# Kernel tuning notes

Hardware: AMD Instinct MI355X
Metric: run time of the kernel (lower is better)

Reference implementation:

```python
import jax, jax.numpy as jnp
import numpy as np
from jax import lax

B, N, C = 8, 8192, 64
ODR, K, OUT = 4, 32, 128
S = N // ODR
EPS = 1e-5


def _lbr(h, W, b, g, be):
    # h: [M, K, Cin] -> linear -> BN (training-mode batch stats over (M,K) per channel) -> relu
    y = jnp.einsum('mki,oi->mko', h, W) + b
    mean = y.mean(axis=(0, 1))
    var = ((y - mean) ** 2).mean(axis=(0, 1))  # biased var, as torch BN uses for normalization
    y = (y - mean) * lax.rsqrt(var + EPS) * g + be
    return jax.nn.relu(y)


def setup_inputs() -> dict:
    key = jax.random.key(0)
    ks = jax.random.split(key, 12)
    x = jax.random.normal(ks[0], (B, N, C), dtype=jnp.float32)
    coor = jax.random.normal(ks[1], (B, N, 3), dtype=jnp.float32)
    indx = jax.random.permutation(ks[2], N)[:S]  # like torch.randperm(N)[:S]
    w1 = jax.random.normal(ks[3], (OUT, 2 * C), dtype=jnp.float32) * (2 * C) ** -0.5
    b1 = jax.random.normal(ks[4], (OUT,), dtype=jnp.float32) * 0.01
    g1 = jax.random.uniform(ks[5], (OUT,), dtype=jnp.float32, minval=0.5, maxval=1.5)
    be1 = jax.random.normal(ks[6], (OUT,), dtype=jnp.float32) * 0.01
    w2 = jax.random.normal(ks[7], (OUT, OUT), dtype=jnp.float32) * OUT ** -0.5
    b2 = jax.random.normal(ks[8], (OUT,), dtype=jnp.float32) * 0.01
    g2 = jax.random.uniform(ks[9], (OUT,), dtype=jnp.float32, minval=0.5, maxval=1.5)
    be2 = jax.random.normal(ks[10], (OUT,), dtype=jnp.float32) * 0.01
    return dict(x=x, coor=coor, indx=indx, w1=w1, b1=b1, g1=g1, be1=be1,
                w2=w2, b2=b2, g2=g2, be2=be2)


def reference(x, coor, indx, w1, b1, g1, be1, w2, b2, g2, be2):
    sampled_coor = coor[:, indx, :]  # [B,S,3]
    sampled_x = x[:, indx, :]        # [B,S,C]
    # pairwise squared distances [B,S,N]
    dist = jnp.sum((coor[:, None, :, :] - sampled_coor[:, :, None, :]) ** 2, axis=-1)
    # k smallest distances == argsort(dist)[..., :K]
    _, knn_idx = lax.top_k(-dist, K)  # [B,S,K]
    knn_x = jax.vmap(lambda xb, ib: xb[ib])(x, knn_idx)  # [B,S,K,C]
    rep_x = jnp.broadcast_to(sampled_x[:, :, None, :], (x.shape[0], S, K, x.shape[2]))
    feat = jnp.concatenate([rep_x, knn_x - rep_x], axis=-1)  # [B,S,K,2C]
    feat = feat.reshape(x.shape[0] * S, K, 2 * x.shape[2])
    h = _lbr(feat, w1, b1, g1, be1)
    h = _lbr(h, w2, b2, g2, be2)
    h = h.reshape(x.shape[0], S, K, -1)
    out = jnp.max(h, axis=2)  # [B,S,OUT]
    return out, sampled_coor
```

## Files before the change

kernel.cpp:

```cpp
#include <hip/hip_runtime.h>
#include <stdint.h>


#define N_    8192
#define GPB_  16

typedef __attribute__((ext_vector_type(8))) short bf8;
typedef __attribute__((ext_vector_type(16))) float f32x16;
typedef __attribute__((ext_vector_type(2))) float f32x2;

__device__ __forceinline__ unsigned int bf1u(float f) {
  unsigned int u = __float_as_uint(f);
  return (u + 0x7fffu + ((u >> 16) & 1u)) >> 16;
}
__device__ __forceinline__ unsigned int bfpair(float lo, float hi) {
  return bf1u(lo) | (bf1u(hi) << 16);
}

__device__ __forceinline__ f32x2 pk_add(f32x2 a, f32x2 b) {
  f32x2 d;
  asm("v_pk_add_f32 %0, %1, %2" : "=v"(d) : "v"(a), "v"(b));
  return d;
}
__device__ __forceinline__ f32x2 pk_mul(f32x2 a, f32x2 b) {
  f32x2 d;
  asm("v_pk_mul_f32 %0, %1, %2" : "=v"(d) : "v"(a), "v"(b));
  return d;
}

__global__ __launch_bounds__(256) void kprep(const float* __restrict__ w1,
                                             const float* __restrict__ w2,
                                             const float* __restrict__ coor,
                                             const int* __restrict__ indx,
                                             unsigned short* __restrict__ w1b,
                                             unsigned short* __restrict__ w2b,
                                             float* __restrict__ outc,
                                             float* __restrict__ soa) {
  int e = blockIdx.x * 256 + threadIdx.x;
  if (e < 16384) {
    w1b[e] = (unsigned short)bf1u(w1[e]);
  } else if (e < 32768) {
    int e2 = e - 16384;
    w2b[e2] = (unsigned short)bf1u(w2[e2]);
  } else if (e < 81920) {
    int e2 = e - 32768;
    int bs = e2 / 3, c = e2 - bs * 3;
    int b = bs >> 11, s = bs & 2047;
    outc[e2] = coor[(b * N_ + indx[s]) * 3 + c];
  } else {
    int p = e - 81920;
    const int b = p >> 13, i = p & 8191;
    const float* src = coor + (size_t)p * 3;
    float* dst = soa + b * 24576;
    dst[i]         = src[0];
    dst[8192 + i]  = src[1];
    dst[16384 + i] = src[2];
  }
}

__global__ __launch_bounds__(256, 8) void kknn(const float* __restrict__ soa,
                                               const int* __restrict__ indx,
                                               int* __restrict__ knn) {
  __shared__ __align__(16) float4 sdist4[4 * 256];
  __shared__ float sTw[8];
  __shared__ unsigned long long cands[192];
  __shared__ int ccnt;

  const int gid = blockIdx.x;
  const int b = gid >> 11, s = gid & 2047;
  const int tid = threadIdx.x;
  const int w = tid >> 6, lane = tid & 63;
  const int hl = lane & 31;
  const float* Xb = soa + b * 24576;
  const float* Yb = Xb + 8192;
  const float* Zb = Xb + 16384;
  const int qi = indx[s];
  const float qx = Xb[qi], qy = Yb[qi], qz = Zb[qi];
  const f32x2 nqx = {-qx, -qx}, nqy = {-qy, -qy}, nqz = {-qz, -qz};

  f32x2 rd[8];
  float dmA = 3.4e38f, dmB = 3.4e38f;
#pragma unroll
  for (int it = 0; it < 8; ++it) {
    const int ofs = (it << 10) + (tid << 2);
    union { float4 f4; f32x2 h[2]; } X, Y, Z;
    X.f4 = *(const float4*)(Xb + ofs);
    Y.f4 = *(const float4*)(Yb + ofs);
    Z.f4 = *(const float4*)(Zb + ofs);
    const f32x2 dxl = pk_add(X.h[0], nqx), dyl = pk_add(Y.h[0], nqy),
                dzl = pk_add(Z.h[0], nqz);
    const f32x2 dxh = pk_add(X.h[1], nqx), dyh = pk_add(Y.h[1], nqy),
                dzh = pk_add(Z.h[1], nqz);
    const f32x2 sl =
        pk_add(pk_add(pk_mul(dxl, dxl), pk_mul(dyl, dyl)), pk_mul(dzl, dzl));
    const f32x2 sh =
        pk_add(pk_add(pk_mul(dxh, dxh), pk_mul(dyh, dyh)), pk_mul(dzh, dzh));
    dmA = fminf(fminf(sl.x, sl.y), dmA);
    dmB = fminf(fminf(sh.x, sh.y), dmB);
    if (it < 4) {
      rd[it * 2] = sl;
      rd[it * 2 + 1] = sh;
    } else {
      union { float4 f4; f32x2 h[2]; } st;
      st.h[0] = sl;
      st.h[1] = sh;
      sdist4[((it - 4) << 8) + tid] = st.f4;
    }
  }
  float dmin = fminf(dmA, dmB);
  if (tid == 0) ccnt = 0;
  if (tid < 192) cands[tid] = ~0ULL;

  float v = dmin;
#pragma unroll
  for (int k = 2; k <= 32; k <<= 1) {
#pragma unroll
    for (int j = k >> 1; j >= 1; j >>= 1) {
      const float o = __shfl_xor(v, j, 64);
      const bool dirAsc = ((hl & k) == 0);
      const bool lower = ((hl & j) == 0);
      const float lo = fminf(v, o), hi = fmaxf(v, o);
      v = (dirAsc == lower) ? lo : hi;
    }
  }
  if (hl == 3) sTw[(w << 1) + (lane >> 5)] = v;
  __syncthreads();
  const float T =
      fmaxf(fmaxf(fmaxf(sTw[0], sTw[1]), fmaxf(sTw[2], sTw[3])),
            fmaxf(fmaxf(sTw[4], sTw[5]), fmaxf(sTw[6], sTw[7])));

#pragma unroll
  for (int t = 0; t < 8; ++t) {
    const int p0 = ((t >> 1) << 10) + (tid << 2) + ((t & 1) << 1);
    const float d0 = rd[t].x, d1 = rd[t].y;
    if (d0 <= T) {
      const int pos = atomicAdd(&ccnt, 1);
      if (pos < 192)
        cands[pos] = ((unsigned long long)__float_as_uint(d0) << 32) |
                     (unsigned int)p0;
    }
    if (d1 <= T) {
      const int pos = atomicAdd(&ccnt, 1);
      if (pos < 192)
        cands[pos] = ((unsigned long long)__float_as_uint(d1) << 32) |
                     (unsigned int)(p0 + 1);
    }
  }
#pragma unroll
  for (int it = 4; it < 8; ++it) {
    const float4 d4 = sdist4[((it - 4) << 8) + tid];
    const int p0 = (it << 10) + (tid << 2);
    const float dd[4] = {d4.x, d4.y, d4.z, d4.w};
#pragma unroll
    for (int j = 0; j < 4; ++j) {
      if (dd[j] <= T) {
        const int pos = atomicAdd(&ccnt, 1);
        if (pos < 192)
          cands[pos] = ((unsigned long long)__float_as_uint(dd[j]) << 32) |
                       (unsigned int)(p0 + j);
      }
    }
  }
  __syncthreads();

  const int E = min(ccnt, 192);
  if (tid < E) {
    const unsigned long long key = cands[tid];
    int rank = 0;
    for (int j = 0; j < E; ++j) rank += (cands[j] < key) ? 1 : 0;
    if (rank < 32) knn[gid * 32 + rank] = (int)(unsigned int)key;
  }
}

template <int PHASE>
__global__ __launch_bounds__(256, 2) void kphase(
    const float* __restrict__ x, const int* __restrict__ indx,
    const int* __restrict__ knn, const float* __restrict__ b1,
    const unsigned short* __restrict__ w1b, const unsigned short* __restrict__ w2b,
    const float* __restrict__ b2, const float* __restrict__ st1,
    float* __restrict__ part, float* __restrict__ mout) {
  __shared__ __align__(16) unsigned short sxb[2][80];
  __shared__ __align__(16) unsigned short dls[2][32 * 68 + 8];
  __shared__ __align__(16) unsigned short h1[PHASE == 2 ? 2 * 32 * 136 : 8];

  const int tid = threadIdx.x;
  const int w = tid >> 6;
  const int lane = tid & 63;
  const int m = lane & 31, q2 = lane >> 5;
  const int col = (w << 5) + m;
  const int r8 = tid >> 3, c8 = (tid & 7) * 8;

  const int bb = blockIdx.x & 7;
  const int jj = blockIdx.x >> 3;
  const float* xb = x + (size_t)bb * (N_ * 64);
  const int gidbase = (bb << 11) + jj * GPB_;
  const int sbase = jj * GPB_;

  bf8 bf1[8];
#pragma unroll
  for (int t = 0; t < 8; ++t)
    bf1[t] = *(const bf8*)&w1b[col * 128 + t * 16 + q2 * 8];
  bf8 bf2[8];
  float s1 = 0.f, t1 = 0.f, b2v = 0.f;
  if constexpr (PHASE == 2) {
#pragma unroll
    for (int t = 0; t < 8; ++t)
      bf2[t] = *(const bf8*)&w2b[col * 128 + t * 16 + q2 * 8];
    s1 = st1[col];
    t1 = st1[128 + col];
    b2v = b2[col];
  }
  (void)w2b; (void)b2; (void)st1; (void)mout;
  const float b1c = b1[col];

  float sum = 0.f, ssq = 0.f;

  float4 ca_c, cc_c, ga_c, gc_c;
  {
    const int idx0 = indx[sbase];
    const int nbr0 = knn[(size_t)gidbase * 32 + r8];
    const float* c0 = xb + (size_t)idx0 * 64;
    ca_c = *(const float4*)(c0 + c8);
    cc_c = *(const float4*)(c0 + c8 + 4);
    const float* g0 = xb + (size_t)nbr0 * 64;
    ga_c = *(const float4*)(g0 + c8);
    gc_c = *(const float4*)(g0 + c8 + 4);
  }
  int idx_nxt = (GPB_ > 1) ? indx[sbase + 1] : 0;
  int nbr_nxt = (GPB_ > 1) ? knn[(size_t)(gidbase + 1) * 32 + r8] : 0;

#pragma unroll 1
  for (int g = 0; g < GPB_; ++g) {
    const int gid = gidbase + g;
    const int p = g & 1;

    float4 ca_n = ca_c, cc_n = cc_c, ga_n = ga_c, gc_n = gc_c;
    if (g + 1 < GPB_) {
      const float* cn = xb + (size_t)idx_nxt * 64;
      ca_n = *(const float4*)(cn + c8);
      cc_n = *(const float4*)(cn + c8 + 4);
      const float* gn = xb + (size_t)nbr_nxt * 64;
      ga_n = *(const float4*)(gn + c8);
      gc_n = *(const float4*)(gn + c8 + 4);
    }
    if (g + 2 < GPB_) {
      nbr_nxt = knn[(size_t)(gid + 2) * 32 + r8];
      idx_nxt = indx[sbase + g + 2];
    }

    {
      uint2 lo, hi;
      lo.x = bfpair(ga_c.x - ca_c.x, ga_c.y - ca_c.y);
      lo.y = bfpair(ga_c.z - ca_c.z, ga_c.w - ca_c.w);
      hi.x = bfpair(gc_c.x - cc_c.x, gc_c.y - cc_c.y);
      hi.y = bfpair(gc_c.z - cc_c.z, gc_c.w - cc_c.w);
      *(uint2*)&dls[p][r8 * 68 + c8] = lo;
      *(uint2*)&dls[p][r8 * 68 + c8 + 4] = hi;
    }
    if (tid < 8) {
      uint2 lo, hi;
      lo.x = bfpair(ca_c.x, ca_c.y);
      lo.y = bfpair(ca_c.z, ca_c.w);
      hi.x = bfpair(cc_c.x, cc_c.y);
      hi.y = bfpair(cc_c.z, cc_c.w);
      *(uint2*)&sxb[p][tid * 8] = lo;
      *(uint2*)&sxb[p][tid * 8 + 4] = hi;
    }
    asm volatile("s_waitcnt lgkmcnt(0)" ::: "memory");
    __builtin_amdgcn_s_barrier();

    bf8 af[8];
#pragma unroll
    for (int t = 0; t < 4; ++t) {
      union { bf8 v; uint2 u[2]; } fa;
      fa.u[0] = *(const uint2*)&sxb[p][t * 16 + q2 * 8];
      fa.u[1] = *(const uint2*)&sxb[p][t * 16 + q2 * 8 + 4];
      af[t] = fa.v;
    }
#pragma unroll
    for (int t = 0; t < 4; ++t) {
      union { bf8 v; uint2 u[2]; } fa;
      fa.u[0] = *(const uint2*)&dls[p][m * 68 + t * 16 + q2 * 8];
      fa.u[1] = *(const uint2*)&dls[p][m * 68 + t * 16 + q2 * 8 + 4];
      af[4 + t] = fa.v;
    }

    f32x16 acc;
#pragma unroll
    for (int r = 0; r < 16; ++r) acc[r] = b1c;
#pragma unroll
    for (int t = 0; t < 8; ++t)
      acc = __builtin_amdgcn_mfma_f32_32x32x16_bf16(af[t], bf1[t], acc, 0, 0, 0);

    if constexpr (PHASE == 1) {
#pragma unroll
      for (int r = 0; r < 16; ++r) {
        const float v = acc[r];
        sum += v;
        ssq = fmaf(v, v, ssq);
      }
    } else {
      const int hp = p * (32 * 136);
#pragma unroll
      for (int r = 0; r < 16; ++r) {
        const float hv = fmaxf(0.f, fmaf(acc[r], s1, t1));
        const int row = (r & 3) + ((r >> 2) << 3) + (q2 << 2);
        h1[hp + row * 136 + col] = (unsigned short)bf1u(hv);
      }
      asm volatile("s_waitcnt lgkmcnt(0)" ::: "memory");
      __builtin_amdgcn_s_barrier();

      f32x16 acc2;
#pragma unroll
      for (int r = 0; r < 16; ++r) acc2[r] = b2v;
#pragma unroll
      for (int t = 0; t < 8; ++t) {
        const bf8 a2 = *(const bf8*)&h1[hp + m * 136 + t * 16 + q2 * 8];
        acc2 = __builtin_amdgcn_mfma_f32_32x32x16_bf16(a2, bf2[t], acc2, 0, 0, 0);
      }

      float mx = -1e30f;
#pragma unroll
      for (int r = 0; r < 16; ++r) {
        const float v = acc2[r];
        sum += v;
        ssq = fmaf(v, v, ssq);
        mx = fmaxf(mx, v);
      }
      mx = fmaxf(mx, __shfl_xor(mx, 32, 64));
      if (lane < 32) mout[(size_t)gid * 128 + col] = mx;
    }

    ca_c = ca_n;
    cc_c = cc_n;
    ga_c = ga_n;
    gc_c = gc_n;
  }

  sum += __shfl_xor(sum, 32, 64);
  ssq += __shfl_xor(ssq, 32, 64);
  if (lane < 32) {
    part[blockIdx.x * 256 + col] = sum;
    part[blockIdx.x * 256 + 128 + col] = ssq;
  }
}

__global__ __launch_bounds__(256) void kred1(const float* __restrict__ part,
                                             double* __restrict__ dbuf) {
  const int blk = blockIdx.x;
  const int c = threadIdx.x;
  const float* p = part + (size_t)blk * 16 * 256 + c;
  double acc = 0.0;
#pragma unroll
  for (int r = 0; r < 16; ++r) acc += (double)p[r * 256];
  dbuf[blk * 256 + c] = acc;
}

__global__ __launch_bounds__(256) void kred2(const double* __restrict__ dbuf,
                                             const float* __restrict__ gam,
                                             const float* __restrict__ bet,
                                             float* __restrict__ st) {
  __shared__ double sS[256];
  const int c = threadIdx.x;
  double acc = 0.0;
#pragma unroll 8
  for (int i = 0; i < 64; ++i) acc += dbuf[i * 256 + c];
  sS[c] = acc;
  __syncthreads();
  if (c < 128) {
    const double Sv = sS[c], SSv = sS[128 + c];
    const double cnt = 524288.0;
    const double mean = Sv / cnt;
    const double var = SSv / cnt - mean * mean;
    const double scale = (double)gam[c] / sqrt(var + 1e-5);
    st[c] = (float)scale;
    st[128 + c] = (float)((double)bet[c] - mean * scale);
  }
}

__global__ __launch_bounds__(256) void kout(const float* __restrict__ m,
                                            const float* __restrict__ st2,
                                            float* __restrict__ out) {
  const int e4 = blockIdx.x * 256 + threadIdx.x;
  const int o0 = (e4 & 31) * 4;
  const float4 v = ((const float4*)m)[e4];
  const float4 sc = *(const float4*)&st2[o0];
  const float4 sh = *(const float4*)&st2[128 + o0];
  float4 r;
  r.x = fmaxf(0.f, fmaf(v.x, sc.x, sh.x));
  r.y = fmaxf(0.f, fmaf(v.y, sc.y, sh.y));
  r.z = fmaxf(0.f, fmaf(v.z, sc.z, sh.z));
  r.w = fmaxf(0.f, fmaf(v.w, sc.w, sh.w));
  ((float4*)out)[e4] = r;
}

extern "C" void kernel_launch(void* const* d_in, const int* in_sizes, int n_in,
                              void* d_out, int out_size, void* d_ws, size_t ws_size,
                              hipStream_t stream) {
  (void)in_sizes; (void)n_in; (void)out_size; (void)ws_size;
  const float* x    = (const float*)d_in[0];
  const float* coor = (const float*)d_in[1];
  const int*   indx = (const int*)d_in[2];
  const float* w1   = (const float*)d_in[3];
  const float* b1   = (const float*)d_in[4];
  const float* g1   = (const float*)d_in[5];
  const float* be1  = (const float*)d_in[6];
  const float* w2   = (const float*)d_in[7];
  const float* b2   = (const float*)d_in[8];
  const float* g2   = (const float*)d_in[9];
  const float* be2  = (const float*)d_in[10];
  float* out = (float*)d_out;

  char* ws = (char*)d_ws;
  int*            knn   = (int*)(ws + 0);
  float*          mbuf  = (float*)(ws + 2097152);
  float*          part1 = (float*)(ws + 10485760);
  float*          soa   = (float*)(ws + 10485760);
  float*          part2 = (float*)(ws + 12582912);
  unsigned short* w1b   = (unsigned short*)(ws + 14680064);
  unsigned short* w2b   = (unsigned short*)(ws + 14712832);
  float*          st1   = (float*)(ws + 14745600);
  float*          st2   = (float*)(ws + 14746624);
  double*         dbuf  = (double*)(ws + 14747648);

  float* outc = out + 2097152;

  kprep<<<576, 256, 0, stream>>>(w1, w2, coor, indx, w1b, w2b, outc, soa);
  kknn<<<16384, 256, 0, stream>>>(soa, indx, knn);
  kphase<1><<<1024, 256, 0, stream>>>(x, indx, knn, b1, w1b, w2b, b2, nullptr,
                                      part1, nullptr);
  kred1<<<64, 256, 0, stream>>>(part1, dbuf);
  kred2<<<1, 256, 0, stream>>>(dbuf, g1, be1, st1);
  kphase<2><<<1024, 256, 0, stream>>>(x, indx, knn, b1, w1b, w2b, b2, st1,
                                      part2, mbuf);
  kred1<<<64, 256, 0, stream>>>(part2, dbuf);
  kred2<<<1, 256, 0, stream>>>(dbuf, g2, be2, st2);
  kout<<<2048, 256, 0, stream>>>(mbuf, st2, out);
}
```

Before: 239.7 us.

## Process two query points per KNN block to reuse coordinate loads

The KNN kernel now handles two sampled query points per block, so each coordinate tile loaded from global memory is reused for two distance computations. The grid is halved, and the selection logic moves into a shared device helper that is called once per query. More distances are held in registers (10 pairs instead of 8) and less shared memory is used per query. In exchange, register pressure rises, launch bounds drop to 4 blocks per SM, and the two selection passes run one after the other.

```diff
diff --git a/kernel.cpp b/kernel.cpp
--- a/kernel.cpp
+++ b/kernel.cpp
@@ -58,28 +58,103 @@
   }
 }
 
-__global__ __launch_bounds__(256, 8) void kknn(const float* __restrict__ soa,
+
+__device__ __forceinline__ void kselect(const float dmin, const f32x2 (&rd)[10],
+                                        const float4* __restrict__ sdq,
+                                        const int gidq, int* __restrict__ knn,
+                                        float* sTw,
+                                        unsigned long long* cands, int* ccnt,
+                                        const int tid, const int w,
+                                        const int lane, const int hl) {
+  __syncthreads();
+  if (tid == 0) *ccnt = 0;
+  if (tid < 192) cands[tid] = ~0ULL;
+
+  float v = dmin;
+#pragma unroll
+  for (int k = 2; k <= 32; k <<= 1) {
+#pragma unroll
+    for (int j = k >> 1; j >= 1; j >>= 1) {
+      const float o = __shfl_xor(v, j, 64);
+      const bool dirAsc = ((hl & k) == 0);
+      const bool lower = ((hl & j) == 0);
+      const float lo = fminf(v, o), hi = fmaxf(v, o);
+      v = (dirAsc == lower) ? lo : hi;
+    }
+  }
+  if (hl == 3) sTw[(w << 1) + (lane >> 5)] = v;
+  __syncthreads();
+  const float T =
+      fmaxf(fmaxf(fmaxf(sTw[0], sTw[1]), fmaxf(sTw[2], sTw[3])),
+            fmaxf(fmaxf(sTw[4], sTw[5]), fmaxf(sTw[6], sTw[7])));
+
+#pragma unroll
+  for (int t = 0; t < 10; ++t) {
+    const int p0 = ((t >> 1) << 10) + (tid << 2) + ((t & 1) << 1);
+    const float d0 = rd[t].x, d1 = rd[t].y;
+    if (d0 <= T) {
+      const int pos = atomicAdd(ccnt, 1);
+      if (pos < 192)
+        cands[pos] = ((unsigned long long)__float_as_uint(d0) << 32) |
+                     (unsigned int)p0;
+    }
+    if (d1 <= T) {
+      const int pos = atomicAdd(ccnt, 1);
+      if (pos < 192)
+        cands[pos] = ((unsigned long long)__float_as_uint(d1) << 32) |
+                     (unsigned int)(p0 + 1);
+    }
+  }
+#pragma unroll
+  for (int it = 5; it < 8; ++it) {
+    const float4 d4 = sdq[((it - 5) << 8) + tid];
+    const int p0 = (it << 10) + (tid << 2);
+    const float dd[4] = {d4.x, d4.y, d4.z, d4.w};
+#pragma unroll
+    for (int j = 0; j < 4; ++j) {
+      if (dd[j] <= T) {
+        const int pos = atomicAdd(ccnt, 1);
+        if (pos < 192)
+          cands[pos] = ((unsigned long long)__float_as_uint(dd[j]) << 32) |
+                       (unsigned int)(p0 + j);
+      }
+    }
+  }
+  __syncthreads();
+
+  const int E = min(*ccnt, 192);
+  if (tid < E) {
+    const unsigned long long key = cands[tid];
+    int rank = 0;
+    for (int j = 0; j < E; ++j) rank += (cands[j] < key) ? 1 : 0;
+    if (rank < 32) knn[gidq * 32 + rank] = (int)(unsigned int)key;
+  }
+}
+
+__global__ __launch_bounds__(256, 4) void kknn(const float* __restrict__ soa,
                                                const int* __restrict__ indx,
                                                int* __restrict__ knn) {
-  __shared__ __align__(16) float4 sdist4[4 * 256];
+  __shared__ __align__(16) float4 sdist4[2][3 * 256];
   __shared__ float sTw[8];
   __shared__ unsigned long long cands[192];
   __shared__ int ccnt;
 
-  const int gid = blockIdx.x;
-  const int b = gid >> 11, s = gid & 2047;
+  const int b = blockIdx.x >> 10;
+  const int s0 = (blockIdx.x & 1023) << 1;
   const int tid = threadIdx.x;
   const int w = tid >> 6, lane = tid & 63;
   const int hl = lane & 31;
   const float* Xb = soa + b * 24576;
   const float* Yb = Xb + 8192;
   const float* Zb = Xb + 16384;
-  const int qi = indx[s];
-  const float qx = Xb[qi], qy = Yb[qi], qz = Zb[qi];
-  const f32x2 nqx = {-qx, -qx}, nqy = {-qy, -qy}, nqz = {-qz, -qz};
-
-  f32x2 rd[8];
-  float dmA = 3.4e38f, dmB = 3.4e38f;
+  const int qi0 = indx[s0], qi1 = indx[s0 + 1];
+  const float qx0 = Xb[qi0], qy0 = Yb[qi0], qz0 = Zb[qi0];
+  const float qx1 = Xb[qi1], qy1 = Yb[qi1], qz1 = Zb[qi1];
+  const f32x2 nqx0 = {-qx0, -qx0}, nqy0 = {-qy0, -qy0}, nqz0 = {-qz0, -qz0};
+  const f32x2 nqx1 = {-qx1, -qx1}, nqy1 = {-qy1, -qy1}, nqz1 = {-qz1, -qz1};
+
+  f32x2 rd0[10], rd1[10];
+  float dmA0 = 3.4e38f, dmB0 = 3.4e38f, dmA1 = 3.4e38f, dmB1 = 3.4e38f;
 #pragma unroll
   for (int it = 0; it < 8; ++it) {
     const int ofs = (it << 10) + (tid << 2);
@@ -87,89 +162,47 @@
     X.f4 = *(const float4*)(Xb + ofs);
     Y.f4 = *(const float4*)(Yb + ofs);
     Z.f4 = *(const float4*)(Zb + ofs);
-    const f32x2 dxl = pk_add(X.h[0], nqx), dyl = pk_add(Y.h[0], nqy),
-                dzl = pk_add(Z.h[0], nqz);
-    const f32x2 dxh = pk_add(X.h[1], nqx), dyh = pk_add(Y.h[1], nqy),
-                dzh = pk_add(Z.h[1], nqz);
-    const f32x2 sl =
-        pk_add(pk_add(pk_mul(dxl, dxl), pk_mul(dyl, dyl)), pk_mul(dzl, dzl));
-    const f32x2 sh =
-        pk_add(pk_add(pk_mul(dxh, dxh), pk_mul(dyh, dyh)), pk_mul(dzh, dzh));
-    dmA = fminf(fminf(sl.x, sl.y), dmA);
-    dmB = fminf(fminf(sh.x, sh.y), dmB);
-    if (it < 4) {
-      rd[it * 2] = sl;
-      rd[it * 2 + 1] = sh;
+    const f32x2 dxl0 = pk_add(X.h[0], nqx0), dyl0 = pk_add(Y.h[0], nqy0),
+                dzl0 = pk_add(Z.h[0], nqz0);
+    const f32x2 dxh0 = pk_add(X.h[1], nqx0), dyh0 = pk_add(Y.h[1], nqy0),
+                dzh0 = pk_add(Z.h[1], nqz0);
+    const f32x2 sl0 =
+        pk_add(pk_add(pk_mul(dxl0, dxl0), pk_mul(dyl0, dyl0)), pk_mul(dzl0, dzl0));
+    const f32x2 sh0 =
+        pk_add(pk_add(pk_mul(dxh0, dxh0), pk_mul(dyh0, dyh0)), pk_mul(dzh0, dzh0));
+    dmA0 = fminf(fminf(sl0.x, sl0.y), dmA0);
+    dmB0 = fminf(fminf(sh0.x, sh0.y), dmB0);
+    const f32x2 dxl1 = pk_add(X.h[0], nqx1), dyl1 = pk_add(Y.h[0], nqy1),
+                dzl1 = pk_add(Z.h[0], nqz1);
+    const f32x2 dxh1 = pk_add(X.h[1], nqx1), dyh1 = pk_add(Y.h[1], nqy1),
+                dzh1 = pk_add(Z.h[1], nqz1);
+    const f32x2 sl1 =
+        pk_add(pk_add(pk_mul(dxl1, dxl1), pk_mul(dyl1, dyl1)), pk_mul(dzl1, dzl1));
+    const f32x2 sh1 =
+        pk_add(pk_add(pk_mul(dxh1, dxh1), pk_mul(dyh1, dyh1)), pk_mul(dzh1, dzh1));
+    dmA1 = fminf(fminf(sl1.x, sl1.y), dmA1);
+    dmB1 = fminf(fminf(sh1.x, sh1.y), dmB1);
+    if (it < 5) {
+      rd0[it * 2] = sl0;
+      rd0[it * 2 + 1] = sh0;
+      rd1[it * 2] = sl1;
+      rd1[it * 2 + 1] = sh1;
     } else {
       union { float4 f4; f32x2 h[2]; } st;
-      st.h[0] = sl;
-      st.h[1] = sh;
-      sdist4[((it - 4) << 8) + tid] = st.f4;
-    }
-  }
-  float dmin = fminf(dmA, dmB);
-  if (tid == 0) ccnt = 0;
-  if (tid < 192) cands[tid] = ~0ULL;
-
-  float v = dmin;
-#pragma unroll
-  for (int k = 2; k <= 32; k <<= 1) {
-#pragma unroll
-    for (int j = k >> 1; j >= 1; j >>= 1) {
-      const float o = __shfl_xor(v, j, 64);
-      const bool dirAsc = ((hl & k) == 0);
-      const bool lower = ((hl & j) == 0);
-      const float lo = fminf(v, o), hi = fmaxf(v, o);
-      v = (dirAsc == lower) ? lo : hi;
-    }
-  }
-  if (hl == 3) sTw[(w << 1) + (lane >> 5)] = v;
-  __syncthreads();
-  const float T =
-      fmaxf(fmaxf(fmaxf(sTw[0], sTw[1]), fmaxf(sTw[2], sTw[3])),
-            fmaxf(fmaxf(sTw[4], sTw[5]), fmaxf(sTw[6], sTw[7])));
-
-#pragma unroll
-  for (int t = 0; t < 8; ++t) {
-    const int p0 = ((t >> 1) << 10) + (tid << 2) + ((t & 1) << 1);
-    const float d0 = rd[t].x, d1 = rd[t].y;
-    if (d0 <= T) {
-      const int pos = atomicAdd(&ccnt, 1);
-      if (pos < 192)
-        cands[pos] = ((unsigned long long)__float_as_uint(d0) << 32) |
-                     (unsigned int)p0;
-    }
-    if (d1 <= T) {
-      const int pos = atomicAdd(&ccnt, 1);
-      if (pos < 192)
-        cands[pos] = ((unsigned long long)__float_as_uint(d1) << 32) |
-                     (unsigned int)(p0 + 1);
-    }
-  }
-#pragma unroll
-  for (int it = 4; it < 8; ++it) {
-    const float4 d4 = sdist4[((it - 4) << 8) + tid];
-    const int p0 = (it << 10) + (tid << 2);
-    const float dd[4] = {d4.x, d4.y, d4.z, d4.w};
-#pragma unroll
-    for (int j = 0; j < 4; ++j) {
-      if (dd[j] <= T) {
-        const int pos = atomicAdd(&ccnt, 1);
-        if (pos < 192)
-          cands[pos] = ((unsigned long long)__float_as_uint(dd[j]) << 32) |
-                       (unsigned int)(p0 + j);
-      }
-    }
-  }
-  __syncthreads();
-
-  const int E = min(ccnt, 192);
-  if (tid < E) {
-    const unsigned long long key = cands[tid];
-    int rank = 0;
-    for (int j = 0; j < E; ++j) rank += (cands[j] < key) ? 1 : 0;
-    if (rank < 32) knn[gid * 32 + rank] = (int)(unsigned int)key;
-  }
+      st.h[0] = sl0;
+      st.h[1] = sh0;
+      sdist4[0][((it - 5) << 8) + tid] = st.f4;
+      st.h[0] = sl1;
+      st.h[1] = sh1;
+      sdist4[1][((it - 5) << 8) + tid] = st.f4;
+    }
+  }
+  const float dmin0 = fminf(dmA0, dmB0);
+  const float dmin1 = fminf(dmA1, dmB1);
+
+  const int gid0 = (b << 11) + s0;
+  kselect(dmin0, rd0, sdist4[0], gid0, knn, sTw, cands, &ccnt, tid, w, lane, hl);
+  kselect(dmin1, rd1, sdist4[1], gid0 + 1, knn, sTw, cands, &ccnt, tid, w, lane, hl);
 }
 
 template <int PHASE>
@@ -426,7 +459,7 @@
   float* outc = out + 2097152;
 
   kprep<<<576, 256, 0, stream>>>(w1, w2, coor, indx, w1b, w2b, outc, soa);
-  kknn<<<16384, 256, 0, stream>>>(soa, indx, knn);
+  kknn<<<8192, 256, 0, stream>>>(soa, indx, knn);
   kphase<1><<<1024, 256, 0, stream>>>(x, indx, knn, b1, w1b, w2b, b2, nullptr,
                                       part1, nullptr);
   kred1<<<64, 256, 0, stream>>>(part1, dbuf);
```

Result: slower. 260.2 us (+8.6%).
